# Performance work log

Hardware: AMD Instinct MI355X
Metric: run time of the kernel (lower is better)

## Reference

```python
import jax, jax.numpy as jnp
import numpy as np

# Regular (dv=3, dc=6) LDPC Tanner graph, rate 1/2
N = 2097152   # variable nodes (code.n)
M = 1048576   # check nodes (H.shape[0])
DV = 3
DC = 6
T = 10        # max_iterations
BC = 4        # c2v bit-width -> 2^(bc-1) = 8 magnitude levels
K = 2 ** (BC - 1)
QUANT_PARAMS = [(2.0, 1.0), (4.0, 1.5), (6.0, 2.0)]


def _make_thresholds():
    """Per-iteration threshold table [T, K]; tau_j = C*(j/(K-1))**gamma."""
    def thr(C, g):
        return [C * (j / (K - 1)) ** g for j in range(K)]
    rows = []
    for t in range(T):
        if t < T // 3:
            C, g = QUANT_PARAMS[0]
        elif t < 2 * T // 3:
            C, g = QUANT_PARAMS[1]
        else:
            C, g = QUANT_PARAMS[-1]
        rows.append(thr(C, g))
    return jnp.asarray(rows, dtype=jnp.float32)


def setup_inputs() -> dict:
    key = jax.random.key(0)
    k_llr, k_beta, k_alpha = jax.random.split(key, 3)
    rng = np.random.default_rng(0)
    # each variable node has exactly DV edges; each check exactly DC edges
    var_idx = np.repeat(np.arange(N, dtype=np.int32), DV)
    chk_idx = rng.permutation(np.repeat(np.arange(M, dtype=np.int32), DC)).astype(np.int32)
    llr = jax.random.normal(k_llr, (N,), dtype=jnp.float32) * 2.0
    # weight init matches nn.Parameter(torch.randn(1)*0.1), one per (iter, degree)
    beta = jax.random.normal(k_beta, (T,), dtype=jnp.float32) * 0.1
    alpha = jax.random.normal(k_alpha, (T,), dtype=jnp.float32) * 0.1
    return {
        "llr": llr,
        "var_idx": jnp.asarray(var_idx),
        "chk_idx": jnp.asarray(chk_idx),
        "beta": beta,
        "alpha": alpha,
        "thresholds": _make_thresholds(),
        "m": M,
    }


def reference(llr, var_idx, chk_idx, beta, alpha, thresholds, m):
    n = llr.shape[0]
    E = var_idx.shape[0]
    eidx = jnp.arange(E, dtype=jnp.int32)
    INF = jnp.float32(jnp.inf)

    def step(v2c, xs):
        b, a, thr = xs  # scalar beta_t, alpha_t, thr [K]
        neg = v2c < 0
        sgn = jnp.where(neg, -1.0, 1.0).astype(v2c.dtype)
        mag = jnp.abs(v2c)
        # --- check node update: min-sum with exclusion (min1/min2) ---
        min1 = jax.ops.segment_min(mag, chk_idx, num_segments=m)
        # first edge attaining the min in each check (ties -> lowest edge id)
        cand = jnp.where(mag <= min1[chk_idx], eidx, E)
        first = jax.ops.segment_min(cand, chk_idx, num_segments=m)
        is_min = eidx == first[chk_idx]
        min2 = jax.ops.segment_min(jnp.where(is_min, INF, mag), chk_idx, num_segments=m)
        min2 = jnp.where(jnp.isinf(min2), min1, min2)  # degree-1 guard
        # sign product excluding self: total parity * own sign
        cnt = jax.ops.segment_sum(neg.astype(jnp.int32), chk_idx, num_segments=m)
        tot = (1 - 2 * (cnt & 1)).astype(v2c.dtype)
        sign_excl = tot[chk_idx] * sgn
        mval = jnp.where(is_min, min2[chk_idx], min1[chk_idx])
        raw = b * sign_excl * mval
        # --- RCQ quantize/dequantize of c2v: snap |raw| down to threshold ---
        q = jnp.clip(jnp.searchsorted(thr, jnp.abs(raw), side="right") - 1, 0, K - 1)
        c2v = jnp.where(raw < 0, -1.0, 1.0) * thr[q]
        # --- variable node update ---
        post = llr + jax.ops.segment_sum(c2v, var_idx, num_segments=n)
        v2c_new = a * (post[var_idx] - c2v)
        return v2c_new, post

    v2c0 = llr[var_idx]
    _, posts = jax.lax.scan(step, v2c0, (beta, alpha, thresholds))
    posterior = posts[-1]
    decoded = (posterior < 0).astype(jnp.int32)
    return decoded, posterior, jnp.int32(beta.shape[0])
```

## Files before the change

kernel.cpp:

```cpp
#include <hip/hip_runtime.h>
#include <stdint.h>

#define NV 2097152
#define MC 1048576
#define EE 6291456
#define TT 10

#define CHUNK 8192
#define NBLK 768
#define FBK 512
#define CPB 2048
#define CSEG 12288
#define FG 512
#define GSEG 12288
#define VBK 256
#define VSEG 24576

__global__ __launch_bounds__(512) void initcur_kernel(uint32_t* __restrict__ gcur) {
    int i = blockIdx.x * 512 + threadIdx.x;
    gcur[i] = (uint32_t)(i & 511) * 12288u;
}

__global__ __launch_bounds__(512) void bin1_kernel(const int* __restrict__ chk_idx,
                                                   uint32_t* __restrict__ gcurA,
                                                   uint32_t* __restrict__ im1_e,
                                                   uint16_t* __restrict__ im1_c) {
    __shared__ uint32_t cnt0[512];
    __shared__ uint32_t aux[512];
    __shared__ uint32_t sA[CHUNK];
    __shared__ uint16_t sB[CHUNK];
    const int tid = threadIdx.x;
    const int rep = tid >> 8;
    const int base = blockIdx.x * CHUNK;
    cnt0[tid] = 0; aux[tid] = 0;
    __syncthreads();
    int4 cc4[4];
#pragma unroll
    for (int k = 0; k < 4; ++k) cc4[k] = ((const int4*)chk_idx)[(base >> 2) + tid + 512 * k];
    uint32_t br[16];
#pragma unroll
    for (int k = 0; k < 4; ++k) {
        int cv[4] = {cc4[k].x, cc4[k].y, cc4[k].z, cc4[k].w};
#pragma unroll
        for (int ii = 0; ii < 4; ++ii) {
            uint32_t b = (uint32_t)cv[ii] >> 11;
            uint32_t r = atomicAdd(rep ? &aux[b] : &cnt0[b], 1u);
            br[k * 4 + ii] = (b << 13) | r;
        }
    }
    __syncthreads();
    const uint32_t s0 = cnt0[tid] + aux[tid];
    aux[tid] = s0;
    __syncthreads();
    for (int d = 1; d < 512; d <<= 1) {
        uint32_t a0 = (tid >= d) ? aux[tid - d] : 0u;
        __syncthreads();
        aux[tid] += a0;
        __syncthreads();
    }
    const uint32_t excl0 = aux[tid] - s0;
    aux[tid] = excl0;
    const uint32_t gb0 = atomicAdd(&gcurA[tid], s0);
    __syncthreads();
#pragma unroll
    for (int k = 0; k < 4; ++k) {
        int cv[4] = {cc4[k].x, cc4[k].y, cc4[k].z, cc4[k].w};
#pragma unroll
        for (int ii = 0; ii < 4; ++ii) {
            uint32_t v = br[k * 4 + ii];
            uint32_t b = v >> 13;
            uint32_t r = v & 8191u;
            uint32_t j = aux[b] + (rep ? cnt0[b] : 0u) + r;
            uint32_t e = (uint32_t)(base + (tid + 512 * k) * 4 + ii);
            sA[j] = (b << 23) | e;
            sB[j] = (uint16_t)((uint32_t)cv[ii] & 2047u);
        }
    }
    __syncthreads();
    aux[tid] = gb0 - excl0;
    __syncthreads();
#pragma unroll 8
    for (int k = 0; k < 16; ++k) {
        int j = tid + 512 * k;
        uint32_t v = sA[j];
        uint32_t b = v >> 23;
        uint32_t addr = aux[b] + (uint32_t)j;
        im1_e[addr] = v & 0x7FFFFFu;
        im1_c[addr] = sB[j];
    }
}

__global__ __launch_bounds__(512) void place1_kernel(const uint32_t* __restrict__ im1_e,
                                                     const uint16_t* __restrict__ im1_c,
                                                     uint32_t* __restrict__ chk_edges,
                                                     uint8_t* __restrict__ b1rank,
                                                     uint32_t* __restrict__ runcntB) {
    __shared__ uint32_t win[CSEG];
    __shared__ uint32_t ccnt[CPB / 2];
    __shared__ uint32_t cntB[VBK];
    const int tid = threadIdx.x, blk = blockIdx.x;
    for (int j = tid; j < CPB / 2; j += 512) ccnt[j] = 0;
    if (tid < VBK) cntB[tid] = 0;
    __syncthreads();
    const size_t cb = (size_t)blk * CSEG;
    for (int k = 0; k < 6; ++k) {
        int j0 = (tid + 512 * k) * 4;
        const uint4 e4 = *(const uint4*)&im1_e[cb + j0];
        const ushort4 c4 = *(const ushort4*)&im1_c[cb + j0];
        uint32_t c, old, s;
        c = c4.x; old = atomicAdd(&ccnt[c >> 1], 1u << ((c & 1) * 16));
        s = (old >> ((c & 1) * 16)) & 0xFFFFu; win[c * 6 + s] = e4.x;
        c = c4.y; old = atomicAdd(&ccnt[c >> 1], 1u << ((c & 1) * 16));
        s = (old >> ((c & 1) * 16)) & 0xFFFFu; win[c * 6 + s] = e4.y;
        c = c4.z; old = atomicAdd(&ccnt[c >> 1], 1u << ((c & 1) * 16));
        s = (old >> ((c & 1) * 16)) & 0xFFFFu; win[c * 6 + s] = e4.z;
        c = c4.w; old = atomicAdd(&ccnt[c >> 1], 1u << ((c & 1) * 16));
        s = (old >> ((c & 1) * 16)) & 0xFFFFu; win[c * 6 + s] = e4.w;
    }
    __syncthreads();
    for (int j = tid; j < CSEG; j += 512) chk_edges[cb + j] = win[j];
    for (int k = 0; k < CSEG / 512; ++k) {
        int lp = tid + 512 * k;
        uint32_t e = win[lp];
        uint32_t bB = (e / 3u) >> 13;
        uint32_t r = atomicAdd(&cntB[bB], 1u);
        b1rank[cb + lp] = (uint8_t)r;
    }
    __syncthreads();
    if (tid < VBK) runcntB[(size_t)tid * FBK + blk] = cntB[tid];
}

__global__ __launch_bounds__(512) void bin2_kernel(const uint32_t* __restrict__ chk_edges,
                                                   uint32_t* __restrict__ gcurB,
                                                   uint32_t* __restrict__ im2_pay,
                                                   uint16_t* __restrict__ im2_el) {
    __shared__ uint32_t cnt0[512];
    __shared__ uint32_t aux[512];
    __shared__ uint32_t sA[CHUNK];
    __shared__ uint16_t sB[CHUNK];
    const int tid = threadIdx.x;
    const int rep = tid >> 8;
    const int base = blockIdx.x * CHUNK;
    cnt0[tid] = 0; aux[tid] = 0;
    __syncthreads();
    uint4 ee4[4];
#pragma unroll
    for (int k = 0; k < 4; ++k) ee4[k] = ((const uint4*)chk_edges)[(base >> 2) + tid + 512 * k];
    uint32_t br[16];
#pragma unroll
    for (int k = 0; k < 4; ++k) {
        uint32_t ev[4] = {ee4[k].x, ee4[k].y, ee4[k].z, ee4[k].w};
#pragma unroll
        for (int ii = 0; ii < 4; ++ii) {
            uint32_t vb = ev[ii] / 12288u;
            uint32_t r = atomicAdd(rep ? &aux[vb] : &cnt0[vb], 1u);
            br[k * 4 + ii] = (vb << 13) | r;
        }
    }
    __syncthreads();
    const uint32_t s0 = cnt0[tid] + aux[tid];
    aux[tid] = s0;
    __syncthreads();
    for (int d = 1; d < 512; d <<= 1) {
        uint32_t a0 = (tid >= d) ? aux[tid - d] : 0u;
        __syncthreads();
        aux[tid] += a0;
        __syncthreads();
    }
    const uint32_t excl0 = aux[tid] - s0;
    aux[tid] = excl0;
    const uint32_t gb0 = atomicAdd(&gcurB[tid], s0);
    __syncthreads();
#pragma unroll
    for (int k = 0; k < 4; ++k) {
        uint32_t ev[4] = {ee4[k].x, ee4[k].y, ee4[k].z, ee4[k].w};
#pragma unroll
        for (int ii = 0; ii < 4; ++ii) {
            uint32_t v = br[k * 4 + ii];
            uint32_t vb = v >> 13;
            uint32_t r = v & 8191u;
            uint32_t j = aux[vb] + (rep ? cnt0[vb] : 0u) + r;
            uint32_t pl = (uint32_t)((tid + 512 * k) * 4 + ii);
            sA[j] = (vb << 13) | pl;
            sB[j] = (uint16_t)(ev[ii] - vb * 12288u);
        }
    }
    __syncthreads();
    aux[tid] = gb0 - excl0;
    __syncthreads();
#pragma unroll 8
    for (int k = 0; k < 16; ++k) {
        int j = tid + 512 * k;
        uint32_t v = sA[j];
        uint32_t vb = v >> 13;
        uint32_t pos = (uint32_t)base + (v & 8191u);
        uint32_t c = pos / 6u;
        uint32_t s = pos - c * 6u;
        uint32_t addr = aux[vb] + (uint32_t)j;
        im2_pay[addr] = (c << 3) | s;
        im2_el[addr] = sB[j];
    }
}

__global__ __launch_bounds__(512) void place2_kernel(const uint32_t* __restrict__ im2_pay,
                                                     const uint16_t* __restrict__ im2_el,
                                                     uint32_t* __restrict__ dest,
                                                     uint8_t* __restrict__ f1rank,
                                                     uint32_t* __restrict__ runcntF) {
    __shared__ uint32_t win2[GSEG];
    __shared__ uint32_t cntF[FBK];
    const int tid = threadIdx.x, g = blockIdx.x;
    cntF[tid] = 0;
    __syncthreads();
    const size_t gb = (size_t)g * GSEG;
    for (int k = 0; k < 6; ++k) {
        int j0 = (tid + 512 * k) * 4;
        const uint4 p4 = *(const uint4*)&im2_pay[gb + j0];
        const ushort4 e4 = *(const ushort4*)&im2_el[gb + j0];
        win2[e4.x] = p4.x; win2[e4.y] = p4.y; win2[e4.z] = p4.z; win2[e4.w] = p4.w;
    }
    __syncthreads();
    for (int j = tid; j < GSEG; j += 512) dest[gb + j] = win2[j];
    for (int k = 0; k < GSEG / 512; ++k) {
        int le = tid + 512 * k;
        uint32_t b = (win2[le] >> 3) >> 11;
        uint32_t r = atomicAdd(&cntF[b], 1u);
        f1rank[gb + le] = (uint8_t)r;
    }
    __syncthreads();
    runcntF[(size_t)tid * FG + g] = cntF[tid];
}

__global__ __launch_bounds__(256) void scanF_kernel(const uint32_t* __restrict__ runcntF,
                                                    uint32_t* __restrict__ f1base) {
    __shared__ uint32_t sc[512];
    const int tid = threadIdx.x, b = blockIdx.x;
    uint32_t c0 = runcntF[(size_t)b * FG + tid];
    uint32_t c1 = runcntF[(size_t)b * FG + tid + 256];
    sc[tid] = c0; sc[tid + 256] = c1;
    __syncthreads();
    for (int d = 1; d < 512; d <<= 1) {
        uint32_t a0 = (tid >= d) ? sc[tid - d] : 0u;
        uint32_t a1 = sc[tid + 256 - d];
        __syncthreads();
        sc[tid] += a0; sc[tid + 256] += a1;
        __syncthreads();
    }
    uint32_t base = (uint32_t)b * CSEG;
    f1base[(size_t)tid * FBK + b] = base + sc[tid] - c0;
    f1base[(size_t)(tid + 256) * FBK + b] = base + sc[tid + 256] - c1;
}

__global__ __launch_bounds__(256) void scanB_kernel(const uint32_t* __restrict__ runcntB,
                                                    uint32_t* __restrict__ b1base) {
    __shared__ uint32_t sc[512];
    const int tid = threadIdx.x, bB = blockIdx.x;
    uint32_t c0 = runcntB[(size_t)bB * FBK + tid];
    uint32_t c1 = runcntB[(size_t)bB * FBK + tid + 256];
    sc[tid] = c0; sc[tid + 256] = c1;
    __syncthreads();
    for (int d = 1; d < 512; d <<= 1) {
        uint32_t a0 = (tid >= d) ? sc[tid - d] : 0u;
        uint32_t a1 = sc[tid + 256 - d];
        __syncthreads();
        sc[tid] += a0; sc[tid + 256] += a1;
        __syncthreads();
    }
    uint32_t base = (uint32_t)bB * VSEG;
    b1base[(size_t)tid * VBK + bB] = base + sc[tid] - c0;
    b1base[(size_t)(tid + 256) * VBK + bB] = base + sc[tid + 256] - c1;
}

__global__ __launch_bounds__(512) void fb_kernel(const uint32_t* __restrict__ dest,
                                                 const uint8_t* __restrict__ f1rank,
                                                 const uint32_t* __restrict__ runcntF,
                                                 const uint32_t* __restrict__ f1base,
                                                 uint32_t* __restrict__ goffF,
                                                 uint16_t* __restrict__ f2pos,
                                                 uint16_t* __restrict__ bidxF,
                                                 uint16_t* __restrict__ lvF) {
    __shared__ uint32_t flb[FBK];
    __shared__ uint32_t rowf[FBK];
    __shared__ uint32_t sortv[GSEG];
    const int tid = threadIdx.x, g = blockIdx.x;
    uint32_t c0 = runcntF[(size_t)tid * FG + g];
    flb[tid] = c0;
    rowf[tid] = f1base[(size_t)g * FBK + tid];
    __syncthreads();
    for (int d = 1; d < FBK; d <<= 1) {
        uint32_t a0 = (tid >= d) ? flb[tid - d] : 0u;
        __syncthreads();
        flb[tid] += a0;
        __syncthreads();
    }
    flb[tid] -= c0;
    __syncthreads();
    goffF[(size_t)g * FBK + tid] = rowf[tid] - flb[tid];
    const size_t gb = (size_t)g * GSEG;
    for (int k = 0; k < GSEG / 512; ++k) {
        int le = tid + 512 * k;
        uint32_t d = dest[gb + le];
        uint32_t r = f1rank[gb + le];
        uint32_t c = d >> 3;
        uint32_t b = c >> 11;
        uint32_t pl = c * 6u + (d & 7u) - b * 12288u;
        sortv[flb[b] + r] = (b << 14) | pl;
    }
    __syncthreads();
    for (int k = 0; k < GSEG / 512; ++k) {
        int j = tid + 512 * k;
        uint32_t v = sortv[j];
        uint32_t b = v >> 14;
        f2pos[rowf[b] - flb[b] + j] = (uint16_t)(v & 16383u);
        bidxF[gb + j] = (uint16_t)b;
    }
    __syncthreads();
    for (int k = 0; k < GSEG / 512; ++k) {
        int le = tid + 512 * k;
        uint32_t d = dest[gb + le];
        uint32_t r = f1rank[gb + le];
        uint32_t b = (d >> 3) >> 11;
        sortv[flb[b] + r] = (uint32_t)(le / 3);
    }
    __syncthreads();
    for (int k = 0; k < GSEG / 512; ++k) {
        int j = tid + 512 * k;
        lvF[gb + j] = (uint16_t)sortv[j];
    }
}

__global__ __launch_bounds__(512) void bb_kernel(const uint32_t* __restrict__ chk_edges,
                                                 const uint8_t* __restrict__ b1rank,
                                                 const uint32_t* __restrict__ runcntB,
                                                 const uint32_t* __restrict__ b1base,
                                                 uint32_t* __restrict__ goffB,
                                                 uint16_t* __restrict__ b2pos,
                                                 uint8_t* __restrict__ bidxB,
                                                 uint16_t* __restrict__ lposB) {
    __shared__ uint32_t blb[VBK];
    __shared__ uint32_t rowb[VBK];
    __shared__ uint32_t sortv[CSEG];
    const int tid = threadIdx.x, blk = blockIdx.x;
    uint32_t c0 = 0;
    if (tid < VBK) {
        c0 = runcntB[(size_t)tid * FBK + blk];
        blb[tid] = c0;
        rowb[tid] = b1base[(size_t)blk * VBK + tid];
    }
    __syncthreads();
    for (int d = 1; d < VBK; d <<= 1) {
        uint32_t a0 = 0;
        if (tid < VBK) a0 = (tid >= d) ? blb[tid - d] : 0u;
        __syncthreads();
        if (tid < VBK) blb[tid] += a0;
        __syncthreads();
    }
    if (tid < VBK) blb[tid] -= c0;
    __syncthreads();
    if (tid < VBK) goffB[(size_t)blk * VBK + tid] = rowb[tid] - blb[tid];
    const size_t cb = (size_t)blk * CSEG;
    for (int k = 0; k < CSEG / 512; ++k) {
        int lp = tid + 512 * k;
        uint32_t e = chk_edges[cb + lp];
        uint32_t r = b1rank[cb + lp];
        uint32_t bB = (e / 3u) >> 13;
        uint32_t elocal = e - bB * VSEG;
        sortv[blb[bB] + r] = (bB << 15) | elocal;
    }
    __syncthreads();
    for (int k = 0; k < CSEG / 512; ++k) {
        int j = tid + 512 * k;
        uint32_t v = sortv[j];
        uint32_t bB = v >> 15;
        b2pos[rowb[bB] - blb[bB] + j] = (uint16_t)(v & 32767u);
        bidxB[cb + j] = (uint8_t)bB;
    }
    __syncthreads();
    for (int k = 0; k < CSEG / 512; ++k) {
        int lp = tid + 512 * k;
        uint32_t e = chk_edges[cb + lp];
        uint32_t r = b1rank[cb + lp];
        uint32_t bB = (e / 3u) >> 13;
        sortv[blb[bB] + r] = (uint32_t)lp;
    }
    __syncthreads();
    for (int k = 0; k < CSEG / 512; ++k) {
        int j = tid + 512 * k;
        lposB[cb + j] = (uint16_t)sortv[j];
    }
}

__global__ __launch_bounds__(512) void check_kernel(const float* __restrict__ finterm,
                                                    const uint16_t* __restrict__ f2pos,
                                                    uint32_t* __restrict__ einfo,
                                                    const uint16_t* __restrict__ lposB,
                                                    const uint8_t* __restrict__ bidxB,
                                                    const uint32_t* __restrict__ goffB,
                                                    uint8_t* __restrict__ binterm,
                                                    const float* __restrict__ beta,
                                                    const float* __restrict__ alpha,
                                                    const float* __restrict__ thresholds,
                                                    int t) {
    __shared__ __align__(16) float fwin[CSEG];
    __shared__ uint32_t grow[VBK];
    __shared__ float tp[8];
    uint32_t* ewin = (uint32_t*)fwin;
    const int tid = threadIdx.x, blk = blockIdx.x;
    if (tid < 8) tp[tid] = thresholds[((t > 0) ? (t - 1) : 0) * 8 + tid];
    if (tid < VBK) grow[tid] = goffB[(size_t)blk * VBK + tid];
    const size_t cb = (size_t)blk * CSEG;
    for (int k = 0; k < 6; ++k) {
        int j0 = (tid + 512 * k) * 4;
        const float4 f4 = *(const float4*)&finterm[cb + j0];
        const ushort4 p4 = *(const ushort4*)&f2pos[cb + j0];
        fwin[p4.x] = f4.x; fwin[p4.y] = f4.y; fwin[p4.z] = f4.z; fwin[p4.w] = f4.w;
    }
    __syncthreads();

    const float aPrev = (t > 0) ? alpha[t - 1] : 1.0f;
    const float b = beta[t];
    const float* thc = thresholds + t * 8;
    const float th1 = thc[1], th2 = thc[2], th3 = thc[3], th4 = thc[4];
    const float th5 = thc[5], th6 = thc[6], th7 = thc[7];
    const uint32_t signb = (b < 0.0f) ? 1u : 0u;

    uint32_t wreg[4];
    for (int i = 0; i < 4; ++i) {
        int lc = tid + 512 * i;
        uint32_t wprev = (t > 0) ? einfo[blk * CPB + lc] : 0u;
        float mags[6];
        uint32_t sgn[6];
        uint32_t parity = 0;
        uint64_t minkey = ~0ull;
#pragma unroll
        for (int j = 0; j < 6; ++j) {
            float p = fwin[lc * 6 + j];
            uint32_t nib = (wprev >> (4 * j)) & 15u;
            float mg0 = tp[nib & 7u];
            float c2v = (nib & 8u) ? -mg0 : mg0;
            float x = aPrev * (p - c2v);
            uint32_t s = (x < 0.0f) ? 1u : 0u;
            parity ^= s;
            sgn[j] = s;
            float mg = fabsf(x);
            mags[j] = mg;
            uint64_t key = (((uint64_t)__float_as_uint(mg)) << 3) | (uint32_t)j;
            minkey = (key < minkey) ? key : minkey;
        }
        float min1 = __uint_as_float((uint32_t)(minkey >> 3));
        uint32_t fs = (uint32_t)(minkey & 7u);
        float min2 = INFINITY;
#pragma unroll
        for (int j = 0; j < 6; ++j) {
            if ((uint32_t)j != fs) min2 = fminf(min2, mags[j]);
        }
        float m1 = fabsf(b * min1);
        float m2 = fabsf(b * min2);
        uint32_t q1 = (uint32_t)(m1 >= th1) + (uint32_t)(m1 >= th2) + (uint32_t)(m1 >= th3)
                    + (uint32_t)(m1 >= th4) + (uint32_t)(m1 >= th5) + (uint32_t)(m1 >= th6)
                    + (uint32_t)(m1 >= th7);
        uint32_t q2 = (uint32_t)(m2 >= th1) + (uint32_t)(m2 >= th2) + (uint32_t)(m2 >= th3)
                    + (uint32_t)(m2 >= th4) + (uint32_t)(m2 >= th5) + (uint32_t)(m2 >= th6)
                    + (uint32_t)(m2 >= th7);
        uint32_t w = 0;
#pragma unroll
        for (int j = 0; j < 6; ++j) {
            uint32_t neg = signb ^ parity ^ sgn[j];
            uint32_t q = ((uint32_t)j == fs) ? q2 : q1;
            w |= ((neg << 3) | q) << (4 * j);
        }
        wreg[i] = w;
    }
    __syncthreads();
    for (int i = 0; i < 4; ++i) {
        int lc = tid + 512 * i;
        ewin[lc] = wreg[i];
        einfo[blk * CPB + lc] = wreg[i];
    }
    __syncthreads();
    for (int k = 0; k < 6; ++k) {
        int j0 = (tid + 512 * k) * 4;
        const ushort4 lp4 = *(const ushort4*)&lposB[cb + j0];
        const uchar4 b4 = *(const uchar4*)&bidxB[cb + j0];
        uint32_t lp, word;
        lp = lp4.x; word = ewin[lp / 6u];
        binterm[grow[b4.x] + j0 + 0] = (uint8_t)((word >> ((lp - 6u * (lp / 6u)) * 4u)) & 15u);
        lp = lp4.y; word = ewin[lp / 6u];
        binterm[grow[b4.y] + j0 + 1] = (uint8_t)((word >> ((lp - 6u * (lp / 6u)) * 4u)) & 15u);
        lp = lp4.z; word = ewin[lp / 6u];
        binterm[grow[b4.z] + j0 + 2] = (uint8_t)((word >> ((lp - 6u * (lp / 6u)) * 4u)) & 15u);
        lp = lp4.w; word = ewin[lp / 6u];
        binterm[grow[b4.w] + j0 + 3] = (uint8_t)((word >> ((lp - 6u * (lp / 6u)) * 4u)) & 15u);
    }
}

__global__ __launch_bounds__(512) void var_kernel(const float* __restrict__ llr,
                                                  const uint8_t* __restrict__ binterm,
                                                  const uint16_t* __restrict__ b2pos,
                                                  const uint16_t* __restrict__ lvF,
                                                  const uint16_t* __restrict__ bidxF,
                                                  const uint32_t* __restrict__ goffF,
                                                  float* __restrict__ finterm,
                                                  const float* __restrict__ thresholds,
                                                  int t, int mode,
                                                  float* __restrict__ out) {
    __shared__ uint8_t nwin[VSEG];
    __shared__ float pwin[4096];
    __shared__ uint32_t growF[FBK];
    __shared__ float tl[8];
    const int tid = threadIdx.x, vblk = blockIdx.x;
    if (tid < 8) tl[tid] = thresholds[t * 8 + tid];
    if (mode != 1) {
        const size_t vb = (size_t)vblk * VSEG;
        for (int k = 0; k < 12; ++k) {
            int i0 = (tid + 512 * k) * 4;
            const uchar4 n4 = *(const uchar4*)&binterm[vb + i0];
            const ushort4 p4 = *(const ushort4*)&b2pos[vb + i0];
            nwin[p4.x] = n4.x; nwin[p4.y] = n4.y; nwin[p4.z] = n4.z; nwin[p4.w] = n4.w;
        }
    }
    __syncthreads();
    for (int h = 0; h < 2; ++h) {
        if (h == 1) __syncthreads();
        for (int i = 0; i < 8; ++i) {
            int lv = tid + 512 * i;
            int lvfull = h * 4096 + lv;
            int v = vblk * 8192 + lvfull;
            float post;
            if (mode == 1) {
                post = llr[v];
            } else {
                uint32_t n0 = nwin[3 * lvfull], n1 = nwin[3 * lvfull + 1], n2 = nwin[3 * lvfull + 2];
                float c0 = (n0 & 8u) ? -tl[n0 & 7u] : tl[n0 & 7u];
                float c1 = (n1 & 8u) ? -tl[n1 & 7u] : tl[n1 & 7u];
                float c2 = (n2 & 8u) ? -tl[n2 & 7u] : tl[n2 & 7u];
                post = llr[v] + ((c0 + c1) + c2);
            }
            pwin[lv] = post;
            if (mode == 2) {
                out[v] = (post < 0.0f) ? 1.0f : 0.0f;
                out[NV + v] = post;
                if (v == 0) out[2 * NV] = 10.0f;
            }
        }
        if (mode == 2) continue;
        const int g = 2 * vblk + h;
        growF[tid] = goffF[(size_t)g * FBK + tid];
        __syncthreads();
        const size_t gb = (size_t)g * GSEG;
        for (int k = 0; k < 6; ++k) {
            int j0 = (tid + 512 * k) * 4;
            const ushort4 lv4 = *(const ushort4*)&lvF[gb + j0];
            const ushort4 b4 = *(const ushort4*)&bidxF[gb + j0];
            finterm[growF[b4.x] + j0 + 0] = pwin[lv4.x];
            finterm[growF[b4.y] + j0 + 1] = pwin[lv4.y];
            finterm[growF[b4.z] + j0 + 2] = pwin[lv4.z];
            finterm[growF[b4.w] + j0 + 3] = pwin[lv4.w];
        }
        __syncthreads();
    }
}

extern "C" void kernel_launch(void* const* d_in, const int* in_sizes, int n_in,
                              void* d_out, int out_size, void* d_ws, size_t ws_size,
                              hipStream_t stream) {
    const float* llr        = (const float*)d_in[0];
    const int*   var_idx    = (const int*)d_in[1];   (void)var_idx;
    const int*   chk_idx    = (const int*)d_in[2];
    const float* beta       = (const float*)d_in[3];
    const float* alpha      = (const float*)d_in[4];
    const float* thresholds = (const float*)d_in[5];
    float* out = (float*)d_out;

    char* wsb = (char*)d_ws;
    float*    finterm   = (float*)(wsb + 0);
    uint16_t* f2pos     = (uint16_t*)(wsb + 25165824);
    uint16_t* lvF       = (uint16_t*)(wsb + 37748736);
    uint16_t* bidxF     = (uint16_t*)(wsb + 50331648);
    uint16_t* lposB     = (uint16_t*)(wsb + 62914560);
    uint16_t* b2pos     = (uint16_t*)(wsb + 75497472);
    uint8_t*  bidxB     = (uint8_t*)(wsb + 88080384);
    uint8_t*  binterm   = (uint8_t*)(wsb + 94371840);
    uint32_t* einfo     = (uint32_t*)(wsb + 100663296);
    uint32_t* chk_edges = (uint32_t*)(wsb + 104857600);
    uint32_t* dest      = (uint32_t*)(wsb + 130023424);
    uint32_t* im1_e     = (uint32_t*)(wsb + 155189248);
    uint16_t* im1_c     = (uint16_t*)(wsb + 180355072);
    uint32_t* im2_pay   = im1_e;
    uint16_t* im2_el    = im1_c;
    uint8_t*  f1rank    = (uint8_t*)(wsb + 192937984);
    uint8_t*  b1rank    = (uint8_t*)(wsb + 199229440);
    uint32_t* runcntF   = (uint32_t*)(wsb + 205520896);
    uint32_t* f1base    = (uint32_t*)(wsb + 206569472);
    uint32_t* runcntB   = (uint32_t*)(wsb + 207618048);
    uint32_t* b1base    = (uint32_t*)(wsb + 208142336);
    uint32_t* goffF     = (uint32_t*)(wsb + 208666624);
    uint32_t* goffB     = (uint32_t*)(wsb + 209715200);
    uint32_t* gcur      = (uint32_t*)(wsb + 210239488);
    uint32_t* gcurA     = gcur;
    uint32_t* gcurB     = gcur + 512;

    initcur_kernel<<<2, 512, 0, stream>>>(gcur);
    bin1_kernel<<<NBLK, 512, 0, stream>>>(chk_idx, gcurA, im1_e, im1_c);
    place1_kernel<<<FBK, 512, 0, stream>>>(im1_e, im1_c, chk_edges, b1rank, runcntB);
    bin2_kernel<<<NBLK, 512, 0, stream>>>(chk_edges, gcurB, im2_pay, im2_el);
    place2_kernel<<<FG, 512, 0, stream>>>(im2_pay, im2_el, dest, f1rank, runcntF);
    scanF_kernel<<<FBK, 256, 0, stream>>>(runcntF, f1base);
    fb_kernel<<<FG, 512, 0, stream>>>(dest, f1rank, runcntF, f1base, goffF, f2pos, bidxF, lvF);
    scanB_kernel<<<VBK, 256, 0, stream>>>(runcntB, b1base);
    bb_kernel<<<FBK, 512, 0, stream>>>(chk_edges, b1rank, runcntB, b1base, goffB, b2pos, bidxB, lposB);
    var_kernel<<<VBK, 512, 0, stream>>>(llr, binterm, b2pos, lvF, bidxF, goffF,
                                        finterm, thresholds, 0, 1, out);

    for (int t = 0; t < TT; ++t) {
        check_kernel<<<FBK, 512, 0, stream>>>(finterm, f2pos, einfo, lposB, bidxB, goffB,
                                              binterm, beta, alpha, thresholds, t);
        var_kernel<<<VBK, 512, 0, stream>>>(llr, binterm, b2pos, lvF, bidxF, goffF,
                                            finterm, thresholds, t,
                                            (t == TT - 1) ? 2 : 0, out);
    }
}
```

Baseline: 692.1 us.

## Compute v2c messages in variable kernel instead of check kernel

```diff
diff --git a/kernel.cpp b/kernel.cpp
--- a/kernel.cpp
+++ b/kernel.cpp
@@ -320,7 +320,9 @@
         uint32_t d = dest[gb + le];
         uint32_t r = f1rank[gb + le];
         uint32_t b = (d >> 3) >> 11;
-        sortv[flb[b] + r] = (uint32_t)(le / 3);
+        uint32_t lv = (uint32_t)(le / 3);
+        uint32_t sl = (uint32_t)le - 3u * lv;
+        sortv[flb[b] + r] = (lv << 2) | sl;
     }
     __syncthreads();
     for (int k = 0; k < GSEG / 512; ++k) {
@@ -392,21 +394,17 @@
 
 __global__ __launch_bounds__(512) void check_kernel(const float* __restrict__ finterm,
                                                     const uint16_t* __restrict__ f2pos,
-                                                    uint32_t* __restrict__ einfo,
                                                     const uint16_t* __restrict__ lposB,
                                                     const uint8_t* __restrict__ bidxB,
                                                     const uint32_t* __restrict__ goffB,
                                                     uint8_t* __restrict__ binterm,
                                                     const float* __restrict__ beta,
-                                                    const float* __restrict__ alpha,
                                                     const float* __restrict__ thresholds,
                                                     int t) {
     __shared__ __align__(16) float fwin[CSEG];
     __shared__ uint32_t grow[VBK];
-    __shared__ float tp[8];
     uint32_t* ewin = (uint32_t*)fwin;
     const int tid = threadIdx.x, blk = blockIdx.x;
-    if (tid < 8) tp[tid] = thresholds[((t > 0) ? (t - 1) : 0) * 8 + tid];
     if (tid < VBK) grow[tid] = goffB[(size_t)blk * VBK + tid];
     const size_t cb = (size_t)blk * CSEG;
     for (int k = 0; k < 6; ++k) {
@@ -417,7 +415,6 @@
     }
     __syncthreads();
 
-    const float aPrev = (t > 0) ? alpha[t - 1] : 1.0f;
     const float b = beta[t];
     const float* thc = thresholds + t * 8;
     const float th1 = thc[1], th2 = thc[2], th3 = thc[3], th4 = thc[4];
@@ -427,18 +424,13 @@
     uint32_t wreg[4];
     for (int i = 0; i < 4; ++i) {
         int lc = tid + 512 * i;
-        uint32_t wprev = (t > 0) ? einfo[blk * CPB + lc] : 0u;
         float mags[6];
         uint32_t sgn[6];
         uint32_t parity = 0;
         uint64_t minkey = ~0ull;
 #pragma unroll
         for (int j = 0; j < 6; ++j) {
-            float p = fwin[lc * 6 + j];
-            uint32_t nib = (wprev >> (4 * j)) & 15u;
-            float mg0 = tp[nib & 7u];
-            float c2v = (nib & 8u) ? -mg0 : mg0;
-            float x = aPrev * (p - c2v);
+            float x = fwin[lc * 6 + j];
             uint32_t s = (x < 0.0f) ? 1u : 0u;
             parity ^= s;
             sgn[j] = s;
@@ -475,7 +467,6 @@
     for (int i = 0; i < 4; ++i) {
         int lc = tid + 512 * i;
         ewin[lc] = wreg[i];
-        einfo[blk * CPB + lc] = wreg[i];
     }
     __syncthreads();
     for (int k = 0; k < 6; ++k) {
@@ -502,6 +493,7 @@
                                                   const uint32_t* __restrict__ goffF,
                                                   float* __restrict__ finterm,
                                                   const float* __restrict__ thresholds,
+                                                  const float* __restrict__ alpha,
                                                   int t, int mode,
                                                   float* __restrict__ out) {
     __shared__ uint8_t nwin[VSEG];
@@ -520,6 +512,7 @@
         }
     }
     __syncthreads();
+    const float a = (mode == 1) ? 1.0f : alpha[t];
     for (int h = 0; h < 2; ++h) {
         if (h == 1) __syncthreads();
         for (int i = 0; i < 8; ++i) {
@@ -545,6 +538,7 @@
         }
         if (mode == 2) continue;
         const int g = 2 * vblk + h;
+        const int hb3 = h * 12288;
         growF[tid] = goffF[(size_t)g * FBK + tid];
         __syncthreads();
         const size_t gb = (size_t)g * GSEG;
@@ -552,10 +546,29 @@
             int j0 = (tid + 512 * k) * 4;
             const ushort4 lv4 = *(const ushort4*)&lvF[gb + j0];
             const ushort4 b4 = *(const ushort4*)&bidxF[gb + j0];
-            finterm[growF[b4.x] + j0 + 0] = pwin[lv4.x];
-            finterm[growF[b4.y] + j0 + 1] = pwin[lv4.y];
-            finterm[growF[b4.z] + j0 + 2] = pwin[lv4.z];
-            finterm[growF[b4.w] + j0 + 3] = pwin[lv4.w];
+            float v0, v1, v2, v3;
+            if (mode == 1) {
+                v0 = pwin[lv4.x >> 2]; v1 = pwin[lv4.y >> 2];
+                v2 = pwin[lv4.z >> 2]; v3 = pwin[lv4.w >> 2];
+            } else {
+                uint32_t e, lvq, nib; float c;
+                e = lv4.x; lvq = e >> 2; nib = nwin[hb3 + 3 * lvq + (e & 3u)];
+                c = (nib & 8u) ? -tl[nib & 7u] : tl[nib & 7u];
+                v0 = a * (pwin[lvq] - c);
+                e = lv4.y; lvq = e >> 2; nib = nwin[hb3 + 3 * lvq + (e & 3u)];
+                c = (nib & 8u) ? -tl[nib & 7u] : tl[nib & 7u];
+                v1 = a * (pwin[lvq] - c);
+                e = lv4.z; lvq = e >> 2; nib = nwin[hb3 + 3 * lvq + (e & 3u)];
+                c = (nib & 8u) ? -tl[nib & 7u] : tl[nib & 7u];
+                v2 = a * (pwin[lvq] - c);
+                e = lv4.w; lvq = e >> 2; nib = nwin[hb3 + 3 * lvq + (e & 3u)];
+                c = (nib & 8u) ? -tl[nib & 7u] : tl[nib & 7u];
+                v3 = a * (pwin[lvq] - c);
+            }
+            finterm[growF[b4.x] + j0 + 0] = v0;
+            finterm[growF[b4.y] + j0 + 1] = v1;
+            finterm[growF[b4.z] + j0 + 2] = v2;
+            finterm[growF[b4.w] + j0 + 3] = v3;
         }
         __syncthreads();
     }
@@ -581,7 +594,6 @@
     uint16_t* b2pos     = (uint16_t*)(wsb + 75497472);
     uint8_t*  bidxB     = (uint8_t*)(wsb + 88080384);
     uint8_t*  binterm   = (uint8_t*)(wsb + 94371840);
-    uint32_t* einfo     = (uint32_t*)(wsb + 100663296);
     uint32_t* chk_edges = (uint32_t*)(wsb + 104857600);
     uint32_t* dest      = (uint32_t*)(wsb + 130023424);
     uint32_t* im1_e     = (uint32_t*)(wsb + 155189248);
@@ -610,13 +622,13 @@
     scanB_kernel<<<VBK, 256, 0, stream>>>(runcntB, b1base);
     bb_kernel<<<FBK, 512, 0, stream>>>(chk_edges, b1rank, runcntB, b1base, goffB, b2pos, bidxB, lposB);
     var_kernel<<<VBK, 512, 0, stream>>>(llr, binterm, b2pos, lvF, bidxF, goffF,
-                                        finterm, thresholds, 0, 1, out);
+                                        finterm, thresholds, alpha, 0, 1, out);
 
     for (int t = 0; t < TT; ++t) {
-        check_kernel<<<FBK, 512, 0, stream>>>(finterm, f2pos, einfo, lposB, bidxB, goffB,
-                                              binterm, beta, alpha, thresholds, t);
+        check_kernel<<<FBK, 512, 0, stream>>>(finterm, f2pos, lposB, bidxB, goffB,
+                                              binterm, beta, thresholds, t);
         var_kernel<<<VBK, 512, 0, stream>>>(llr, binterm, b2pos, lvF, bidxF, goffF,
-                                            finterm, thresholds, t,
+                                            finterm, thresholds, alpha, t,
                                             (t == TT - 1) ? 2 : 0, out);
     }
 }
```

New measurement: 641.8 us. 1.08x faster.
